# Kernel optimization log

Hardware: AMD Instinct MI355X
Metric: run time of the kernel (lower is better)

Reference implementation:

```python
import jax, jax.numpy as jnp
import numpy as np

N_NEIGHBORS = 16
NEIGHBOR_LIMIT = 20
N_BINS = 5
EPS = 1e-12


def _distance_matrix(coords):
    # coords: (N, 3) -> (N, N) pairwise Euclidean distances
    sq = jnp.sum(coords * coords, axis=-1)
    dm = sq[:, None] - 2.0 * (coords @ coords.T) + sq[None, :]
    return jnp.sqrt(jnp.abs(dm))


def _shot_lrf(nbh, radius):
    # nbh: (N, K, 3) local neighbor coordinates. SHOT local reference frames.
    d = jnp.linalg.norm(nbh, axis=-1)                       # (N, K)
    w = jnp.maximum(radius - d, 0.0)                        # SHOT distance weights
    cov = jnp.einsum("nk,nki,nkj->nij", w, nbh, nbh)
    cov = cov / (jnp.sum(w, axis=-1)[:, None, None] + EPS)  # (N, 3, 3)
    _, eigvecs = jnp.linalg.eigh(cov)                       # ascending eigenvalues
    x_axes = eigvecs[:, :, 2]                               # largest eigenvalue
    z_axes = eigvecs[:, :, 0]                               # smallest eigenvalue (normal)

    def disambiguate(axes):
        dots = jnp.einsum("nki,ni->nk", nbh, axes)
        pos = jnp.sum((dots >= 0.0).astype(jnp.float32), axis=-1)
        neg = jnp.sum((dots < 0.0).astype(jnp.float32), axis=-1)
        sign = jnp.where(pos >= neg, 1.0, -1.0)
        return axes * sign[:, None]

    x_axes = disambiguate(x_axes)
    z_axes = disambiguate(z_axes)
    y_axes = jnp.cross(z_axes, x_axes)
    return jnp.stack([x_axes, y_axes, z_axes], axis=1)      # (N, 3, 3)


def _log_map(lrfs, nbh):
    # project local neighbors onto tangent plane, preserving vector length
    u = jnp.einsum("nki,ni->nk", nbh, lrfs[:, 0])
    v = jnp.einsum("nki,ni->nk", nbh, lrfs[:, 1])
    plane = jnp.stack([u, v], axis=-1)                      # (N, K, 2)
    norms = jnp.linalg.norm(nbh, axis=-1)
    plane_norms = jnp.linalg.norm(plane, axis=-1)
    return plane * (norms / (plane_norms + EPS))[..., None]


def _histograms(proj, radius, n_bins):
    # proj: (N, K, 2) tangent-plane projections -> (N, n_bins**2) normalized histograms
    step = 2.0 * radius / n_bins
    c = jnp.linspace(-radius, radius, n_bins + 1)[:-1] + step / 2.0
    weights = radius - jnp.sqrt(c[:, None] ** 2 + c[None, :] ** 2)  # (n_bins, n_bins)

    bins = jnp.floor((proj + radius) / step)                # (N, K, 2)
    valid = jnp.all((bins >= 0.0) & (bins < n_bins), axis=-1)
    bx = jnp.clip(bins[..., 0].astype(jnp.int32), 0, n_bins - 1)
    by = jnp.clip(bins[..., 1].astype(jnp.int32), 0, n_bins - 1)
    flat = by * n_bins + bx                                 # hist[row=y_bin, col=x_bin]
    n_pts = flat.shape[0]
    b2 = n_bins * n_bins
    offset = jnp.arange(n_pts)[:, None] * b2
    hist = jnp.zeros((n_pts * b2,), jnp.float32).at[(offset + flat).reshape(-1)].add(
        valid.reshape(-1).astype(jnp.float32))
    hist = hist.reshape(n_pts, n_bins, n_bins) * weights[None]
    hist = hist / jnp.linalg.norm(hist, axis=(1, 2), keepdims=True)
    return hist.reshape(n_pts, b2)


def _single_cloud(coords):
    dm = _distance_matrix(coords)
    order = jnp.argsort(dm, axis=-1)
    dsort = jnp.take_along_axis(dm, order, axis=-1)
    radius = jnp.mean(dsort[:, N_NEIGHBORS])
    nbr_idx = order[:, :NEIGHBOR_LIMIT]
    nbr_dist = dsort[:, :NEIGHBOR_LIMIT]
    nbh = coords[nbr_idx] - coords[:, None, :]              # (N, K, 3) local coords
    fill = (2.0 * radius) / jnp.sqrt(3.0)                   # dummy coord of length 2*radius
    nbh = jnp.where((nbr_dist > radius)[..., None], fill, nbh)
    lrfs = _shot_lrf(nbh, radius)
    proj = _log_map(lrfs, nbh)
    return _histograms(proj, radius, N_BINS)


def setup_inputs() -> dict:
    key = jax.random.key(0)
    batched_coordinates = jax.random.normal(key, (4, 4096, 3), dtype=jnp.float32)
    return {"batched_coordinates": batched_coordinates}


def reference(batched_coordinates):
    return jax.vmap(_single_cloud)(batched_coordinates)
```

## Files before the change

### kernel.cpp

```cpp
#include <hip/hip_runtime.h>
#include <math.h>

#pragma clang fp contract(off)

#define NPTS 4096
#define NBATCH 4
#define NTOT (NBATCH * NPTS)
#define NNB 20
#define NBINS 5
#define LTOP 7

#define SEPS    5.9604644775390625e-8f
#define SSAFMIN 1.17549435e-38f


__device__ __forceinline__ float f_signf(float a, float b) {
  return __builtin_signbit(b) ? -fabsf(a) : fabsf(a);
}

__device__ float slapy2_(float x, float y) {
  float xa = fabsf(x), ya = fabsf(y);
  float w = fmaxf(xa, ya), z = fminf(xa, ya);
  if (z == 0.0f) return w;
  float t = z / w;
  return w * sqrtf(1.0f + t * t);
}

__device__ void slartg_(float f, float g, float* c, float* s, float* r) {
  if (g == 0.0f) {
    *c = 1.0f; *s = 0.0f; *r = f;
  } else if (f == 0.0f) {
    *c = 0.0f; *s = __builtin_signbit(g) ? -1.0f : 1.0f; *r = fabsf(g);
  } else {
    float f1 = fabsf(f);
    float d = sqrtf(f * f + g * g);
    *c = f1 / d;
    float rr = __builtin_signbit(f) ? -d : d;
    *r = rr;
    *s = g / rr;
  }
}

__device__ void slaev2_(float a, float b, float c,
                        float* rt1, float* rt2, float* cs1, float* sn1) {
  float sm = a + c;
  float df = a - c;
  float adf = fabsf(df);
  float tb = b + b;
  float ab = fabsf(tb);
  float acmx, acmn;
  if (fabsf(a) > fabsf(c)) { acmx = a; acmn = c; } else { acmx = c; acmn = a; }
  float rt;
  if (adf > ab)      { float t = ab / adf; rt = adf * sqrtf(1.0f + t * t); }
  else if (adf < ab) { float t = adf / ab; rt = ab * sqrtf(1.0f + t * t); }
  else               { rt = ab * sqrtf(2.0f); }
  int sgn1;
  if (sm < 0.0f) {
    *rt1 = 0.5f * (sm - rt); sgn1 = -1;
    *rt2 = (acmx / *rt1) * acmn - (b / *rt1) * b;
  } else if (sm > 0.0f) {
    *rt1 = 0.5f * (sm + rt); sgn1 = 1;
    *rt2 = (acmx / *rt1) * acmn - (b / *rt1) * b;
  } else {
    *rt1 = 0.5f * rt; *rt2 = -0.5f * rt; sgn1 = 1;
  }
  float cs; int sgn2;
  if (df >= 0.0f) { cs = df + rt; sgn2 = 1; }
  else            { cs = df - rt; sgn2 = -1; }
  float acs = fabsf(cs);
  float csv, snv;
  if (acs > ab) {
    float ct = -tb / cs;
    snv = 1.0f / sqrtf(1.0f + ct * ct);
    csv = ct * snv;
  } else {
    if (ab == 0.0f) { csv = 1.0f; snv = 0.0f; }
    else {
      float tn = -cs / tb;
      csv = 1.0f / sqrtf(1.0f + tn * tn);
      snv = tn * csv;
    }
  }
  if (sgn1 == sgn2) { float tn = csv; csv = -snv; snv = tn; }
  *cs1 = csv; *sn1 = snv;
}

#define DD(i)    w[(i) * 64]
#define EE(i)    w[(3 + (i)) * 64]
#define ZZ(i, j) w[(5 + (i) * 3 + (j)) * 64]
#define CC(i)    w[(14 + (i)) * 64]
#define SN(i)    w[(16 + (i)) * 64]

__device__ void ssteqr3_lds(float* w) {
  const int n = 3;
  const float eps = SEPS;
  const float eps2 = SEPS * SEPS;
  const float safmin = SSAFMIN;
  const int nmaxit = 90;
  int jtot = 0;
  int l1 = 1;
  int l = 0, lsv = 0, lend = 0, lendsv = 0, m = 0, mm = 0;
  float p = 0, g = 0, r = 0, c = 0, s = 0, f = 0, bb = 0, rt1 = 0, rt2 = 0;
  float anorm = 0, tst = 0;

L10:
  if (l1 > n) goto L160;
  if (l1 > 1) EE(l1 - 2) = 0.0f;
  if (l1 <= n - 1) {
    for (m = l1; m <= n - 1; ++m) {
      tst = fabsf(EE(m - 1));
      if (tst == 0.0f) goto L30;
      if (tst <= (sqrtf(fabsf(DD(m - 1))) * sqrtf(fabsf(DD(m)))) * eps) {
        EE(m - 1) = 0.0f;
        goto L30;
      }
    }
  }
  m = n;
L30:
  l = l1; lsv = l; lend = m; lendsv = lend; l1 = m + 1;
  if (lend == l) goto L10;
  anorm = 0.0f;
  for (int i = l; i <= lend; ++i) anorm = fmaxf(anorm, fabsf(DD(i - 1)));
  for (int i = l; i <= lend - 1; ++i) anorm = fmaxf(anorm, fabsf(EE(i - 1)));
  if (anorm == 0.0f) goto L10;
  if (fabsf(DD(lend - 1)) < fabsf(DD(l - 1))) { lend = lsv; l = lendsv; }

  if (lend > l) {
L40:
    if (l != lend) {
      for (m = l; m <= lend - 1; ++m) {
        tst = EE(m - 1) * EE(m - 1);
        if (tst <= (eps2 * fabsf(DD(m - 1))) * fabsf(DD(m)) + safmin) goto L60;
      }
    }
    m = lend;
L60:
    if (m < lend) EE(m - 1) = 0.0f;
    p = DD(l - 1);
    if (m == l) goto L80;
    if (m == l + 1) {
      slaev2_(DD(l - 1), EE(l - 1), DD(l), &rt1, &rt2, &c, &s);
      for (int i = 0; i < n; ++i) {
        float tz = ZZ(i, l);
        ZZ(i, l)     = c * tz - s * ZZ(i, l - 1);
        ZZ(i, l - 1) = s * tz + c * ZZ(i, l - 1);
      }
      DD(l - 1) = rt1; DD(l) = rt2; EE(l - 1) = 0.0f;
      l += 2;
      if (l <= lend) goto L40;
      goto L140;
    }
    if (jtot == nmaxit) goto L140;
    jtot++;
    g = (DD(l) - p) / (2.0f * EE(l - 1));
    r = slapy2_(g, 1.0f);
    g = DD(m - 1) - p + EE(l - 1) / (g + f_signf(r, g));
    s = 1.0f; c = 1.0f; p = 0.0f;
    for (int i = m - 1; i >= l; --i) {
      f = s * EE(i - 1);
      bb = c * EE(i - 1);
      slartg_(g, f, &c, &s, &r);
      if (i != m - 1) EE(i) = r;
      g = DD(i) - p;
      r = (DD(i - 1) - g) * s + 2.0f * c * bb;
      p = s * r;
      DD(i) = g + p;
      g = c * r - bb;
      CC(i - 1) = c; SN(i - 1) = -s;
    }
    mm = m - l + 1;
    for (int j = mm - 1; j >= 1; --j) {
      float ct = CC(l + j - 2), st = SN(l + j - 2);
      for (int i = 0; i < n; ++i) {
        float tz = ZZ(i, l + j - 1);
        ZZ(i, l + j - 1) = ct * tz - st * ZZ(i, l + j - 2);
        ZZ(i, l + j - 2) = st * tz + ct * ZZ(i, l + j - 2);
      }
    }
    DD(l - 1) -= p;
    EE(l - 1) = g;
    goto L40;
L80:
    DD(l - 1) = p;
    l++;
    if (l <= lend) goto L40;
    goto L140;
  } else {
L90:
    if (l != lend) {
      for (m = l; m >= lend + 1; --m) {
        tst = EE(m - 2) * EE(m - 2);
        if (tst <= (eps2 * fabsf(DD(m - 1))) * fabsf(DD(m - 2)) + safmin) goto L110;
      }
    }
    m = lend;
L110:
    if (m > lend) EE(m - 2) = 0.0f;
    p = DD(l - 1);
    if (m == l) goto L130;
    if (m == l - 1) {
      slaev2_(DD(l - 2), EE(l - 2), DD(l - 1), &rt1, &rt2, &c, &s);
      for (int i = 0; i < n; ++i) {
        float tz = ZZ(i, l - 1);
        ZZ(i, l - 1) = c * tz - s * ZZ(i, l - 2);
        ZZ(i, l - 2) = s * tz + c * ZZ(i, l - 2);
      }
      DD(l - 2) = rt1; DD(l - 1) = rt2; EE(l - 2) = 0.0f;
      l -= 2;
      if (l >= lend) goto L90;
      goto L140;
    }
    if (jtot == nmaxit) goto L140;
    jtot++;
    g = (DD(l - 2) - p) / (2.0f * EE(l - 2));
    r = slapy2_(g, 1.0f);
    g = DD(m - 1) - p + EE(l - 2) / (g + f_signf(r, g));
    s = 1.0f; c = 1.0f; p = 0.0f;
    for (int i = m; i <= l - 1; ++i) {
      f = s * EE(i - 1);
      bb = c * EE(i - 1);
      slartg_(g, f, &c, &s, &r);
      if (i != m) EE(i - 2) = r;
      g = DD(i - 1) - p;
      r = (DD(i) - g) * s + 2.0f * c * bb;
      p = s * r;
      DD(i - 1) = g + p;
      g = c * r - bb;
      CC(i - 1) = c; SN(i - 1) = s;
    }
    mm = l - m + 1;
    for (int j = 1; j <= mm - 1; ++j) {
      float ct = CC(m + j - 2), st = SN(m + j - 2);
      for (int i = 0; i < n; ++i) {
        float tz = ZZ(i, m + j - 1);
        ZZ(i, m + j - 1) = ct * tz - st * ZZ(i, m + j - 2);
        ZZ(i, m + j - 2) = st * tz + ct * ZZ(i, m + j - 2);
      }
    }
    DD(l - 1) -= p;
    EE(l - 2) = g;
    goto L90;
L130:
    DD(l - 1) = p;
    l--;
    if (l >= lend) goto L90;
    goto L140;
  }
L140:
  if (jtot < nmaxit) goto L10;
  goto L160;
L160:
  for (int ii = 2; ii <= n; ++ii) {
    int i = ii - 1, k = i;
    float pp = DD(i - 1);
    for (int j = ii; j <= n; ++j)
      if (DD(j - 1) < pp) { k = j; pp = DD(j - 1); }
    if (k != i) {
      DD(k - 1) = DD(i - 1); DD(i - 1) = pp;
      for (int row = 0; row < n; ++row) {
        float t2 = ZZ(row, i - 1); ZZ(row, i - 1) = ZZ(row, k - 1); ZZ(row, k - 1) = t2;
      }
    }
  }
}

__device__ void eigh3f_lds(float A00, float A10, float A20, float A11, float A21, float A22,
                           float* w, float V[3][3]) {
  float taui, v2, beta;
  float alpha = A10;
  float xnorm = fabsf(A20);
  if (xnorm == 0.0f) {
    taui = 0.0f; beta = alpha; v2 = 0.0f;
  } else {
    beta = -f_signf(slapy2_(alpha, xnorm), alpha);
    taui = (beta - alpha) / beta;
    v2 = A20 * (1.0f / (alpha - beta));
  }
  float a11 = A11, a21 = A21, a22 = A22;
  if (taui != 0.0f) {
    float w0 = taui * (a11 + a21 * v2);
    float w1 = taui * (a21 + a22 * v2);
    float al = -0.5f * taui * (w0 + w1 * v2);
    w0 += al; w1 += al * v2;
    a11 -= 2.0f * w0;
    a21 -= (v2 * w0 + w1);
    a22 -= 2.0f * (v2 * w1);
  }
  DD(0) = A00; DD(1) = a11; DD(2) = a22;
  EE(0) = beta; EE(1) = a21;
  ZZ(0, 0) = 1.0f; ZZ(0, 1) = 0.0f; ZZ(0, 2) = 0.0f;
  ZZ(1, 0) = 0.0f; ZZ(1, 1) = 1.0f; ZZ(1, 2) = 0.0f;
  ZZ(2, 0) = 0.0f; ZZ(2, 1) = 0.0f; ZZ(2, 2) = 1.0f;

  ssteqr3_lds(w);

  for (int k = 0; k < 3; ++k) {
    float t = taui * (ZZ(1, k) + v2 * ZZ(2, k));
    ZZ(1, k) -= t;
    ZZ(2, k) -= t * v2;
  }
  for (int i = 0; i < 3; ++i)
    for (int k = 0; k < 3; ++k) V[i][k] = ZZ(i, k);
}

__device__ __forceinline__ unsigned wave_min_dpp(unsigned v) {
  unsigned t;
  t = (unsigned)__builtin_amdgcn_update_dpp(-1, (int)v, 0x111, 0xf, 0xf, false); v = t < v ? t : v;
  t = (unsigned)__builtin_amdgcn_update_dpp(-1, (int)v, 0x112, 0xf, 0xf, false); v = t < v ? t : v;
  t = (unsigned)__builtin_amdgcn_update_dpp(-1, (int)v, 0x114, 0xf, 0xf, false); v = t < v ? t : v;
  t = (unsigned)__builtin_amdgcn_update_dpp(-1, (int)v, 0x118, 0xf, 0xf, false); v = t < v ? t : v;
  t = (unsigned)__builtin_amdgcn_update_dpp(-1, (int)v, 0x142, 0xa, 0xf, false); v = t < v ? t : v;
  t = (unsigned)__builtin_amdgcn_update_dpp(-1, (int)v, 0x143, 0xc, 0xf, false); v = t < v ? t : v;
  return v;
}


__global__ __launch_bounds__(1024, 8) void knn_kernel(const float* __restrict__ coords,
                                                      float* __restrict__ nbrD,
                                                      int* __restrict__ nbrI,
                                                      float* __restrict__ d16) {
  __shared__ float4 scs[NPTS];
  int tid = threadIdx.x;
  int wid = tid >> 6;
  int lane = tid & 63;
  int P = blockIdx.x * 16 + wid;
  int b = P >> 12;
  int p = P & (NPTS - 1);
  const float* cb = coords + (size_t)b * NPTS * 3;

  for (int i = tid; i < NPTS; i += 1024) {
    float x = cb[3 * i + 0], y = cb[3 * i + 1], z = cb[3 * i + 2];
    float sq = (x * x + y * y) + z * z;
    scs[i] = make_float4(x, y, z, sq);
  }
  __syncthreads();

  float4 ci = scs[p];
  float xi = ci.x, yi = ci.y, zi = ci.z, sqi = ci.w;

  const double INF = __hiloint2double(0x7FF00000, 0);
  double L[LTOP];
#pragma unroll
  for (int t = 0; t < LTOP; ++t) L[t] = INF;

#pragma unroll 8
  for (int k = 0; k < NPTS / 64; ++k) {
    int j = k * 64 + lane;
    float4 cj = scs[j];
    float dot = (xi * cj.x + yi * cj.y) + zi * cj.z;
    float d2 = (sqi - 2.0f * dot) + cj.w;
    unsigned kb = __float_as_uint(d2) & 0x7FFFFFFFu;
    double cur = __hiloint2double((int)kb, j);
    double m1 = fmax(cur, L[0]);
    double m2 = fmax(cur, L[1]);
    double m3 = fmax(cur, L[2]);
    double m4 = fmax(cur, L[3]);
    double m5 = fmax(cur, L[4]);
    double m6 = fmax(cur, L[5]);
    L[0] = fmin(L[0], cur);
    L[1] = fmin(L[1], m1);
    L[2] = fmin(L[2], m2);
    L[3] = fmin(L[3], m3);
    L[4] = fmin(L[4], m4);
    L[5] = fmin(L[5], m5);
    L[6] = fmin(L[6], m6);
  }

  unsigned resHi = 0, resLo = 0;
  for (int r = 0; r < NNB; ++r) {
    unsigned hi0 = (unsigned)__double2hiint(L[0]);
    unsigned lo0 = (unsigned)__double2loint(L[0]);
    unsigned gh = wave_min_dpp(hi0);
    gh = (unsigned)__builtin_amdgcn_readlane((int)gh, 63);
    unsigned lom = (hi0 == gh) ? lo0 : 0xFFFFFFFFu;
    unsigned gl = wave_min_dpp(lom);
    gl = (unsigned)__builtin_amdgcn_readlane((int)gl, 63);
    bool mine = (hi0 == gh) && (lo0 == gl);
#pragma unroll
    for (int t = 0; t < LTOP - 1; ++t) L[t] = mine ? L[t + 1] : L[t];
    L[LTOP - 1] = mine ? INF : L[LTOP - 1];
    if (lane == r) { resHi = gh; resLo = gl; }
  }

  if (lane < NNB) {
    float dist = sqrtf(__uint_as_float(resHi));
    nbrD[(size_t)lane * NTOT + P] = dist;
    nbrI[(size_t)lane * NTOT + P] = (int)resLo;
    if (lane == 16) d16[P] = dist;
  }
}


__global__ __launch_bounds__(64) void shot_kernel(const float* __restrict__ coords,
                                                  const float* __restrict__ d16,
                                                  const float* __restrict__ nbrD,
                                                  const int* __restrict__ nbrI,
                                                  float* __restrict__ out) {
  __shared__ float buf[NPTS];
  __shared__ float ews[18 * 64];
  int lane = threadIdx.x;
  int g = blockIdx.x * 64 + lane;
  int b = g >> 12;
  int p = g & (NPTS - 1);
  const float* cb = coords + (size_t)b * NPTS * 3;

  for (int i = lane; i < NPTS; i += 64) buf[i] = d16[(size_t)b * NPTS + i];

  int jj[NNB];
  float dd[NNB];
#pragma unroll
  for (int k = 0; k < NNB; ++k) {
    jj[k] = nbrI[(size_t)k * NTOT + g];
    dd[k] = nbrD[(size_t)k * NTOT + g];
  }
  float gx[NNB], gy[NNB], gz[NNB];
#pragma unroll
  for (int k = 0; k < NNB; ++k) {
    int j = jj[k];
    gx[k] = cb[j * 3 + 0];
    gy[k] = cb[j * 3 + 1];
    gz[k] = cb[j * 3 + 2];
  }
  float xi = cb[p * 3 + 0], yi = cb[p * 3 + 1], zi = cb[p * 3 + 2];

  __syncthreads();
  float s = 0.0f;
  for (int k = 0; k < NPTS; ++k) s += buf[k];
  float radius = s / 4096.0f;

  float fill = 2.0f * radius / sqrtf(3.0f);

  float nbx[NNB], nby[NNB], nbz[NNB], dk[NNB];
#pragma unroll
  for (int k = 0; k < NNB; ++k) {
    float nx, ny, nz;
    if (dd[k] > radius) { nx = fill; ny = fill; nz = fill; }
    else {
      nx = gx[k] - xi;
      ny = gy[k] - yi;
      nz = gz[k] - zi;
    }
    nbx[k] = nx; nby[k] = ny; nbz[k] = nz;
    dk[k] = sqrtf((nx * nx + ny * ny) + nz * nz);
  }

  float wsum = 0.0f;
  float c00 = 0, c11 = 0, c22 = 0;
  float c01 = 0, c10 = 0, c02 = 0, c20 = 0, c12 = 0, c21 = 0;
  for (int k = 0; k < NNB; ++k) {
    float w = fmaxf(radius - dk[k], 0.0f);
    wsum += w;
    float wx = w * nbx[k], wy = w * nby[k], wz = w * nbz[k];
    c00 += wx * nbx[k]; c01 += wx * nby[k]; c02 += wx * nbz[k];
    c10 += wy * nbx[k]; c11 += wy * nby[k]; c12 += wy * nbz[k];
    c20 += wz * nbx[k]; c21 += wz * nby[k]; c22 += wz * nbz[k];
  }
  float den = wsum + 1e-12f;
  float a00 = c00 / den, a11 = c11 / den, a22 = c22 / den;
  float a01 = c01 / den, a10 = c10 / den;
  float a02 = c02 / den, a20 = c20 / den;
  float a12 = c12 / den, a21 = c21 / den;
  float A10 = 0.5f * (a01 + a10);
  float A20 = 0.5f * (a02 + a20);
  float A21 = 0.5f * (a12 + a21);

  float V[3][3];
  eigh3f_lds(a00, A10, A20, a11, A21, a22, &ews[lane], V);

  float xax0 = V[0][2], xax1 = V[1][2], xax2 = V[2][2];
  float zax0 = V[0][0], zax1 = V[1][0], zax2 = V[2][0];

  {
    int pos = 0, neg = 0;
    for (int k = 0; k < NNB; ++k) {
      float dt = (nbx[k] * xax0 + nby[k] * xax1) + nbz[k] * xax2;
      if (dt >= 0.0f) pos++; else neg++;
    }
    if (pos < neg) { xax0 = -xax0; xax1 = -xax1; xax2 = -xax2; }
  }
  {
    int pos = 0, neg = 0;
    for (int k = 0; k < NNB; ++k) {
      float dt = (nbx[k] * zax0 + nby[k] * zax1) + nbz[k] * zax2;
      if (dt >= 0.0f) pos++; else neg++;
    }
    if (pos < neg) { zax0 = -zax0; zax1 = -zax1; zax2 = -zax2; }
  }
  float yax0 = zax1 * xax2 - zax2 * xax1;
  float yax1 = zax2 * xax0 - zax0 * xax2;
  float yax2 = zax0 * xax1 - zax1 * xax0;

  float hist[NBINS * NBINS];
  for (int k = 0; k < NBINS * NBINS; ++k) hist[k] = 0.0f;
  float stp = 2.0f * radius / (float)NBINS;
  for (int k = 0; k < NNB; ++k) {
    float u = (nbx[k] * xax0 + nby[k] * xax1) + nbz[k] * xax2;
    float v = (nbx[k] * yax0 + nby[k] * yax1) + nbz[k] * yax2;
    float pn = sqrtf(u * u + v * v);
    float sc = dk[k] / (pn + 1e-12f);
    float pu = u * sc, pv = v * sc;
    float bxf = floorf((pu + radius) / stp);
    float byf = floorf((pv + radius) / stp);
    if (bxf >= 0.0f && bxf < (float)NBINS && byf >= 0.0f && byf < (float)NBINS) {
      int bx = (int)bxf, by = (int)byf;
      hist[by * NBINS + bx] += 1.0f;
    }
  }
  float cvals[NBINS];
  for (int i = 0; i < NBINS; ++i) cvals[i] = ((float)i * stp - radius) + 0.5f * stp;
  float nrm2 = 0.0f;
  for (int i = 0; i < NBINS; ++i) {
    for (int j = 0; j < NBINS; ++j) {
      float wgt = radius - sqrtf(cvals[i] * cvals[i] + cvals[j] * cvals[j]);
      float h = hist[i * NBINS + j] * wgt;
      hist[i * NBINS + j] = h;
      nrm2 += h * h;
    }
  }
  float nrm = sqrtf(nrm2);
  for (int k = 0; k < NBINS * NBINS; ++k) {
    out[(size_t)g * (NBINS * NBINS) + k] = hist[k] / nrm;
  }
}


extern "C" void kernel_launch(void* const* d_in, const int* in_sizes, int n_in,
                              void* d_out, int out_size, void* d_ws, size_t ws_size,
                              hipStream_t stream) {
  const float* coords = (const float*)d_in[0];
  float* out = (float*)d_out;

  float* wsf = (float*)d_ws;
  float* d16 = wsf + 8;
  float* nbrD = wsf + 8 + (size_t)NTOT;
  int* nbrI = (int*)(nbrD + (size_t)NNB * NTOT);

  knn_kernel<<<NTOT / 16, 1024, 0, stream>>>(coords, nbrD, nbrI, d16);
  shot_kernel<<<NTOT / 64, 64, 0, stream>>>(coords, d16, nbrD, nbrI, out);
}
```

Baseline: 117.0 us.

## Shrink SHOT blocks to 8 threads and move histogram into shared memory

The SHOT kernel now launches 8-thread blocks instead of 64, so the grid has 2048 blocks instead of 256 and more CUs get work. The per-thread histogram, which was dynamically indexed and likely spilled to scratch, now lives in LDS with an 8-float stride, and the eigen-solver workspace stride shrinks to match. The radius reduction reads d16 straight from global memory instead of staging it in LDS, so every thread sums 4096 values through the cache. That adds redundant global traffic, and 8-thread blocks leave most of each 64-wide wavefront idle.

```diff
diff --git a/kernel.cpp b/kernel.cpp
--- a/kernel.cpp
+++ b/kernel.cpp
@@ -9,6 +9,7 @@
 #define NNB 20
 #define NBINS 5
 #define LTOP 7
+#define WST 8
 
 #define SEPS    5.9604644775390625e-8f
 #define SSAFMIN 1.17549435e-38f
@@ -85,11 +86,11 @@
   *cs1 = csv; *sn1 = snv;
 }
 
-#define DD(i)    w[(i) * 64]
-#define EE(i)    w[(3 + (i)) * 64]
-#define ZZ(i, j) w[(5 + (i) * 3 + (j)) * 64]
-#define CC(i)    w[(14 + (i)) * 64]
-#define SN(i)    w[(16 + (i)) * 64]
+#define DD(i)    w[(i) * WST]
+#define EE(i)    w[(3 + (i)) * WST]
+#define ZZ(i, j) w[(5 + (i) * 3 + (j)) * WST]
+#define CC(i)    w[(14 + (i)) * WST]
+#define SN(i)    w[(16 + (i)) * WST]
 
 __device__ void ssteqr3_lds(float* w) {
   const int n = 3;
@@ -397,15 +398,14 @@
                                                   const float* __restrict__ nbrD,
                                                   const int* __restrict__ nbrI,
                                                   float* __restrict__ out) {
-  __shared__ float buf[NPTS];
-  __shared__ float ews[18 * 64];
+  __shared__ float ews[18 * WST];
+  __shared__ float hws[25 * WST];
   int lane = threadIdx.x;
-  int g = blockIdx.x * 64 + lane;
+  int g = blockIdx.x * WST + lane;
   int b = g >> 12;
   int p = g & (NPTS - 1);
   const float* cb = coords + (size_t)b * NPTS * 3;
-
-  for (int i = lane; i < NPTS; i += 64) buf[i] = d16[(size_t)b * NPTS + i];
+  const float* d16b = d16 + (size_t)b * NPTS;
 
   int jj[NNB];
   float dd[NNB];
@@ -424,9 +424,8 @@
   }
   float xi = cb[p * 3 + 0], yi = cb[p * 3 + 1], zi = cb[p * 3 + 2];
 
-  __syncthreads();
   float s = 0.0f;
-  for (int k = 0; k < NPTS; ++k) s += buf[k];
+  for (int k = 0; k < NPTS; ++k) s += d16b[k];
   float radius = s / 4096.0f;
 
   float fill = 2.0f * radius / sqrtf(3.0f);
@@ -491,8 +490,9 @@
   float yax1 = zax2 * xax0 - zax0 * xax2;
   float yax2 = zax0 * xax1 - zax1 * xax0;
 
-  float hist[NBINS * NBINS];
-  for (int k = 0; k < NBINS * NBINS; ++k) hist[k] = 0.0f;
+  float* hh = &hws[lane];
+#pragma unroll
+  for (int k = 0; k < NBINS * NBINS; ++k) hh[k * WST] = 0.0f;
   float stp = 2.0f * radius / (float)NBINS;
   for (int k = 0; k < NNB; ++k) {
     float u = (nbx[k] * xax0 + nby[k] * xax1) + nbz[k] * xax2;
@@ -504,23 +504,28 @@
     float byf = floorf((pv + radius) / stp);
     if (bxf >= 0.0f && bxf < (float)NBINS && byf >= 0.0f && byf < (float)NBINS) {
       int bx = (int)bxf, by = (int)byf;
-      hist[by * NBINS + bx] += 1.0f;
+      hh[(by * NBINS + bx) * WST] += 1.0f;
     }
   }
   float cvals[NBINS];
+#pragma unroll
   for (int i = 0; i < NBINS; ++i) cvals[i] = ((float)i * stp - radius) + 0.5f * stp;
   float nrm2 = 0.0f;
+  float hreg[NBINS * NBINS];
+#pragma unroll
   for (int i = 0; i < NBINS; ++i) {
+#pragma unroll
     for (int j = 0; j < NBINS; ++j) {
       float wgt = radius - sqrtf(cvals[i] * cvals[i] + cvals[j] * cvals[j]);
-      float h = hist[i * NBINS + j] * wgt;
-      hist[i * NBINS + j] = h;
+      float h = hh[(i * NBINS + j) * WST] * wgt;
+      hreg[i * NBINS + j] = h;
       nrm2 += h * h;
     }
   }
   float nrm = sqrtf(nrm2);
+#pragma unroll
   for (int k = 0; k < NBINS * NBINS; ++k) {
-    out[(size_t)g * (NBINS * NBINS) + k] = hist[k] / nrm;
+    out[(size_t)g * (NBINS * NBINS) + k] = hreg[k] / nrm;
   }
 }
 
@@ -537,5 +542,5 @@
   int* nbrI = (int*)(nbrD + (size_t)NNB * NTOT);
 
   knn_kernel<<<NTOT / 16, 1024, 0, stream>>>(coords, nbrD, nbrI, d16);
-  shot_kernel<<<NTOT / 64, 64, 0, stream>>>(coords, d16, nbrD, nbrI, out);
-}
+  shot_kernel<<<NTOT / WST, WST, 0, stream>>>(coords, d16, nbrD, nbrI, out);
+}
```

New measurement: 179.3 us. 53.3% more time.
